# Performance work log

Measured on AMD Instinct MI355X. Metric: run time of the kernel, lower is better.

Reference implementation:

```python
import jax, jax.numpy as jnp
import numpy as np
import math

B, S, D_IN, D_OUT = 4, 2048, 1024, 1024
NEG = -1000000000.0


def setup_inputs() -> dict:
    key = jax.random.key(0)
    ks = jax.random.split(key, 8)
    scale = 1.0 / math.sqrt(D_IN)
    return {
        "x": jax.random.normal(ks[0], (B, S, D_IN), dtype=jnp.float32),
        "Wq": jax.random.normal(ks[1], (D_OUT, D_IN), dtype=jnp.float32) * scale,
        "bq": jax.random.normal(ks[2], (D_OUT,), dtype=jnp.float32) * scale,
        "Wk": jax.random.normal(ks[3], (D_OUT, D_IN), dtype=jnp.float32) * scale,
        "bk": jax.random.normal(ks[4], (D_OUT,), dtype=jnp.float32) * scale,
        "Wv": jax.random.normal(ks[5], (D_OUT, D_IN), dtype=jnp.float32) * scale,
        "bv": jax.random.normal(ks[6], (D_OUT,), dtype=jnp.float32) * scale,
        "lengths": jax.random.randint(ks[7], (B,), 1, S + 1, dtype=jnp.int32),
    }


def reference(x, Wq, bq, Wk, bk, Wv, bv, lengths):
    # QKV projections (self-attention: single input used for q, k, v)
    q = jnp.einsum("bsd,od->bso", x, Wq) + bq
    k = jnp.einsum("bsd,od->bso", x, Wk) + bk
    v = jnp.einsum("bsd,od->bso", x, Wv) + bv
    # scaled scores [B, S, S]
    scores = jnp.einsum("bio,bjo->bij", q, k) / jnp.sqrt(jnp.asarray(D_OUT, q.dtype))
    idx = jnp.arange(S)
    # causal additive mask (mask=True): -1e9 where j > i
    causal = jnp.where(idx[None, :] > idx[:, None], NEG, 0.0).astype(q.dtype)
    # length mask: -1e9 where i >= len[b] or j >= len[b]
    invalid = idx[None, :] >= lengths[:, None]  # [B, S]
    len_mask = jnp.where(invalid[:, :, None] | invalid[:, None, :], NEG, 0.0).astype(q.dtype)
    attn = jax.nn.softmax(scores + causal[None] + len_mask, axis=-1)
    return jnp.einsum("bij,bjo->bio", attn, v)
```

## Files before the change

kernel.cpp:

```cpp
#include <hip/hip_runtime.h>
#include <cstddef>
#include <cstdint>

#define NB 4
#define S_LEN 2048
#define DK 1024

typedef __attribute__((ext_vector_type(8))) short short8;
typedef __attribute__((ext_vector_type(4))) float floatx4;
typedef __attribute__((ext_vector_type(4))) unsigned short ushort4v;
typedef __attribute__((ext_vector_type(8))) unsigned short ushort8v;

__device__ inline unsigned short f2bf(float f) {
    unsigned int u = __float_as_uint(f);
    u += 0x7fff + ((u >> 16) & 1);
    return (unsigned short)(u >> 16);
}
__device__ inline float bf2f(unsigned short u) {
    return __uint_as_float(((unsigned int)u) << 16);
}

#define GLD16(gp, lp)                                                                  \
    __builtin_amdgcn_global_load_lds(                                                  \
        (const __attribute__((address_space(1))) unsigned int*)(gp),                   \
        (__attribute__((address_space(3))) unsigned int*)(lp), 16, 0, 0)

__device__ inline void stage128x64(const unsigned short* __restrict__ g, size_t ld,
                                   unsigned short* __restrict__ lds,
                                   int w, int lane)
{
    const int r8 = lane >> 3;
    const int cg = (lane & 7) ^ r8;
    const unsigned short* gp = g + (size_t)(w * 8 + r8) * ld + cg * 8;
    unsigned short* lp = lds + (size_t)(w * 8) * 64;
    #pragma unroll
    for (int seg = 0; seg < 4; ++seg)
        GLD16(gp + (size_t)(seg * 32) * ld, lp + (size_t)seg * 32 * 64);
}

__global__ __launch_bounds__(256) void cast_all(
    const float* __restrict__ x, const float* __restrict__ Wq,
    const float* __restrict__ Wk, const float* __restrict__ Wv,
    unsigned short* __restrict__ xb, unsigned short* __restrict__ wqb,
    unsigned short* __restrict__ wkb, unsigned short* __restrict__ wvb)
{
    const float* src; unsigned short* dst; int n4;
    if (blockIdx.z == 0)      { src = x;  dst = xb;  n4 = (int)((size_t)NB * S_LEN * DK / 4); }
    else if (blockIdx.z == 1) { src = Wq; dst = wqb; n4 = DK * DK / 4; }
    else if (blockIdx.z == 2) { src = Wk; dst = wkb; n4 = DK * DK / 4; }
    else                      { src = Wv; dst = wvb; n4 = DK * DK / 4; }
    const int stride = gridDim.x * 256;
    for (int i = blockIdx.x * 256 + threadIdx.x; i < n4; i += stride) {
        float4 f = ((const float4*)src)[i];
        ushort4v o;
        o.x = f2bf(f.x); o.y = f2bf(f.y); o.z = f2bf(f.z); o.w = f2bf(f.w);
        ((ushort4v*)dst)[i] = o;
    }
}

__global__ __launch_bounds__(256) void qkv_mfma(
    const unsigned short* __restrict__ xb,
    const unsigned short* __restrict__ wqb, const unsigned short* __restrict__ wkb,
    const unsigned short* __restrict__ wvb,
    const float* __restrict__ bq, const float* __restrict__ bk, const float* __restrict__ bv,
    unsigned short* __restrict__ qb, unsigned short* __restrict__ kb,
    unsigned short* __restrict__ vTb)
{
    __shared__ unsigned short As[128 * 64];
    __shared__ unsigned short Bs[128 * 64];
    const int tid  = threadIdx.x;
    const int w    = tid >> 6, lane = tid & 63;
    const int lm   = lane & 15, quad = lane >> 4;
    const int xr   = lm & 7;
    const int m0   = blockIdx.x * 128, n0 = blockIdx.y * 128;
    const int z    = blockIdx.z;
    const unsigned short* Wb = (z == 0) ? wqb : (z == 1) ? wkb : wvb;
    const float* bias        = (z == 0) ? bq  : (z == 1) ? bk  : bv;

    const unsigned short* Ag = xb + (size_t)m0 * DK;
    const unsigned short* Bg = Wb + (size_t)n0 * DK;

    const int wr = (w >> 1) * 64, wc = (w & 1) * 64;

    floatx4 acc[4][4];
    #pragma unroll
    for (int r = 0; r < 4; ++r)
        #pragma unroll
        for (int c = 0; c < 4; ++c) acc[r][c] = (floatx4)0.0f;

    for (int k0 = 0; k0 < DK; k0 += 64) {
        stage128x64(Ag + k0, DK, As, w, lane);
        stage128x64(Bg + k0, DK, Bs, w, lane);
        __syncthreads();
        #pragma unroll
        for (int ks = 0; ks < 2; ++ks) {
            short8 af[4], bf[4];
            #pragma unroll
            for (int r = 0; r < 4; ++r)
                af[r] = *(const short8*)&As[(size_t)(wr + r*16 + lm) * 64 + ((((ks<<2)|quad) ^ xr) << 3)];
            #pragma unroll
            for (int c = 0; c < 4; ++c)
                bf[c] = *(const short8*)&Bs[(size_t)(wc + c*16 + lm) * 64 + ((((ks<<2)|quad) ^ xr) << 3)];
            #pragma unroll
            for (int r = 0; r < 4; ++r)
                #pragma unroll
                for (int c = 0; c < 4; ++c)
                    acc[r][c] = __builtin_amdgcn_mfma_f32_16x16x32_bf16(af[r], bf[c], acc[r][c], 0, 0, 0);
        }
        __syncthreads();
    }

    if (z < 2) {
        unsigned short* out = (z == 0) ? qb : kb;
        #pragma unroll
        for (int r = 0; r < 4; ++r) {
            const int gm = m0 + wr + r * 16 + quad * 4;
            #pragma unroll
            for (int c = 0; c < 4; ++c) {
                const int gn = n0 + wc + c * 16 + lm;
                const float bb = bias[gn];
                #pragma unroll
                for (int e = 0; e < 4; ++e)
                    out[(size_t)(gm + e) * DK + gn] = f2bf(acc[r][c][e] + bb);
            }
        }
    } else {
        const int bidx = m0 >> 11;
        #pragma unroll
        for (int r = 0; r < 4; ++r) {
            const int gm = m0 + wr + r * 16 + quad * 4;
            const int sm = gm & (S_LEN - 1);
            #pragma unroll
            for (int c = 0; c < 4; ++c) {
                const int gn = n0 + wc + c * 16 + lm;
                const float bb = bias[gn];
                ushort4v pk;
                pk.x = f2bf(acc[r][c][0] + bb);
                pk.y = f2bf(acc[r][c][1] + bb);
                pk.z = f2bf(acc[r][c][2] + bb);
                pk.w = f2bf(acc[r][c][3] + bb);
                *(ushort4v*)&vTb[((size_t)bidx * DK + gn) * S_LEN + sm] = pk;
            }
        }
    }
}

__global__ __launch_bounds__(256) void score_mfma(
    const unsigned short* __restrict__ qb, const unsigned short* __restrict__ kb,
    unsigned short* __restrict__ Pf)
{
    const int bi = blockIdx.x, bj = blockIdx.y, b = blockIdx.z;
    if (bj > bi) return;
    const int m0 = bi * 128, n0 = bj * 128;

    __shared__ unsigned short As[128 * 64];
    __shared__ unsigned short Bs[128 * 64];
    const int tid  = threadIdx.x;
    const int w    = tid >> 6, lane = tid & 63;
    const int lm   = lane & 15, quad = lane >> 4;
    const int xr   = lm & 7;
    const unsigned short* Ag = qb + (size_t)b * S_LEN * DK + (size_t)m0 * DK;
    const unsigned short* Bg = kb + (size_t)b * S_LEN * DK + (size_t)n0 * DK;
    unsigned short* Pb_ = Pf + (size_t)b * S_LEN * S_LEN;

    const int wr = (w >> 1) * 64, wc = (w & 1) * 64;

    floatx4 acc[4][4];
    #pragma unroll
    for (int r = 0; r < 4; ++r)
        #pragma unroll
        for (int c = 0; c < 4; ++c) acc[r][c] = (floatx4)0.0f;

    for (int k0 = 0; k0 < DK; k0 += 64) {
        stage128x64(Ag + k0, DK, As, w, lane);
        stage128x64(Bg + k0, DK, Bs, w, lane);
        __syncthreads();
        #pragma unroll
        for (int ks = 0; ks < 2; ++ks) {
            short8 af[4], bf[4];
            #pragma unroll
            for (int r = 0; r < 4; ++r)
                af[r] = *(const short8*)&As[(size_t)(wr + r*16 + lm) * 64 + ((((ks<<2)|quad) ^ xr) << 3)];
            #pragma unroll
            for (int c = 0; c < 4; ++c)
                bf[c] = *(const short8*)&Bs[(size_t)(wc + c*16 + lm) * 64 + ((((ks<<2)|quad) ^ xr) << 3)];
            #pragma unroll
            for (int r = 0; r < 4; ++r)
                #pragma unroll
                for (int c = 0; c < 4; ++c)
                    acc[r][c] = __builtin_amdgcn_mfma_f32_16x16x32_bf16(af[r], bf[c], acc[r][c], 0, 0, 0);
        }
        __syncthreads();
    }

    #pragma unroll
    for (int r = 0; r < 4; ++r) {
        const int gm = m0 + wr + r * 16 + quad * 4;
        #pragma unroll
        for (int c = 0; c < 4; ++c) {
            const int gn = n0 + wc + c * 16 + lm;
            #pragma unroll
            for (int e = 0; e < 4; ++e)
                Pb_[(size_t)(gm + e) * S_LEN + gn] = f2bf(acc[r][c][e] * 0.03125f);
        }
    }
}

__global__ __launch_bounds__(256) void softmax_rows(
    const unsigned short* __restrict__ Pf, unsigned short* __restrict__ Pb,
    const int* __restrict__ lengths)
{
    const int row = blockIdx.x;
    const int b = row >> 11, i = row & (S_LEN - 1);
    const unsigned short* p = Pf + (size_t)row * S_LEN;
    unsigned short* o = Pb + (size_t)row * S_LEN;
    const int len = lengths[b];
    const int t = threadIdx.x;
    const int nv = i + 1;
    const int j0 = t * 8;

    if (i >= len) {
        const unsigned short u = f2bf(1.0f / (float)nv);
        ushort8v pk;
        #pragma unroll
        for (int e = 0; e < 8; ++e) pk[e] = (j0 + e < nv) ? u : (unsigned short)0;
        *(ushort8v*)&o[j0] = pk;
        return;
    }

    float v[8];
    float m = -INFINITY;
    if (j0 < nv) {
        ushort8v raw = *(const ushort8v*)&p[j0];
        #pragma unroll
        for (int e = 0; e < 8; ++e) {
            float xv = (j0 + e < nv) ? bf2f(raw[e]) : -INFINITY;
            v[e] = xv;
            m = fmaxf(m, xv);
        }
    } else {
        #pragma unroll
        for (int e = 0; e < 8; ++e) v[e] = -INFINITY;
    }

    __shared__ float red[256];
    red[t] = m; __syncthreads();
    #pragma unroll
    for (int s2 = 128; s2 > 0; s2 >>= 1) {
        if (t < s2) red[t] = fmaxf(red[t], red[t + s2]);
        __syncthreads();
    }
    const float M = red[0];
    __syncthreads();

    float s = 0.0f;
    #pragma unroll
    for (int e = 0; e < 8; ++e) {
        if (j0 + e < nv) { v[e] = __expf(v[e] - M); s += v[e]; }
        else v[e] = 0.0f;
    }
    red[t] = s; __syncthreads();
    #pragma unroll
    for (int s2 = 128; s2 > 0; s2 >>= 1) {
        if (t < s2) red[t] += red[t + s2];
        __syncthreads();
    }
    const float inv = 1.0f / red[0];

    ushort8v pk;
    #pragma unroll
    for (int e = 0; e < 8; ++e) pk[e] = f2bf(v[e] * inv);
    *(ushort8v*)&o[j0] = pk;
}

__global__ __launch_bounds__(256) void pv_mfma(
    const unsigned short* __restrict__ Pb, const unsigned short* __restrict__ vTb,
    float* __restrict__ out)
{
    __shared__ unsigned short As[128 * 64];
    __shared__ unsigned short Bs[128 * 64];
    const int tid  = threadIdx.x;
    const int w    = tid >> 6, lane = tid & 63;
    const int lm   = lane & 15, quad = lane >> 4;
    const int xr   = lm & 7;
    const int bi = blockIdx.x, bn = blockIdx.y, b = blockIdx.z;
    const int m0 = bi * 128, n0 = bn * 128;
    const unsigned short* Ag = Pb  + (size_t)b * S_LEN * S_LEN + (size_t)m0 * S_LEN;
    const unsigned short* Bg = vTb + (size_t)b * DK * S_LEN    + (size_t)n0 * S_LEN;

    const int wr = (w >> 1) * 64, wc = (w & 1) * 64;
    const int kend = (bi + 1) * 128;

    floatx4 acc[4][4];
    #pragma unroll
    for (int r = 0; r < 4; ++r)
        #pragma unroll
        for (int c = 0; c < 4; ++c) acc[r][c] = (floatx4)0.0f;

    for (int k0 = 0; k0 < kend; k0 += 64) {
        stage128x64(Ag + k0, S_LEN, As, w, lane);
        stage128x64(Bg + k0, S_LEN, Bs, w, lane);
        __syncthreads();
        #pragma unroll
        for (int ks = 0; ks < 2; ++ks) {
            short8 af[4], bf[4];
            #pragma unroll
            for (int r = 0; r < 4; ++r)
                af[r] = *(const short8*)&As[(size_t)(wr + r*16 + lm) * 64 + ((((ks<<2)|quad) ^ xr) << 3)];
            #pragma unroll
            for (int c = 0; c < 4; ++c)
                bf[c] = *(const short8*)&Bs[(size_t)(wc + c*16 + lm) * 64 + ((((ks<<2)|quad) ^ xr) << 3)];
            #pragma unroll
            for (int r = 0; r < 4; ++r)
                #pragma unroll
                for (int c = 0; c < 4; ++c)
                    acc[r][c] = __builtin_amdgcn_mfma_f32_16x16x32_bf16(af[r], bf[c], acc[r][c], 0, 0, 0);
        }
        __syncthreads();
    }

    #pragma unroll
    for (int r = 0; r < 4; ++r) {
        const int gm = m0 + wr + r * 16 + quad * 4;
        #pragma unroll
        for (int c = 0; c < 4; ++c) {
            const int gn = n0 + wc + c * 16 + lm;
            #pragma unroll
            for (int e = 0; e < 4; ++e)
                out[((size_t)b * S_LEN + gm + e) * DK + gn] = acc[r][c][e];
        }
    }
}

extern "C" void kernel_launch(void* const* d_in, const int* in_sizes, int n_in,
                              void* d_out, int out_size, void* d_ws, size_t ws_size,
                              hipStream_t stream)
{
    const float* x  = (const float*)d_in[0];
    const float* Wq = (const float*)d_in[1];
    const float* bq = (const float*)d_in[2];
    const float* Wk = (const float*)d_in[3];
    const float* bk = (const float*)d_in[4];
    const float* Wv = (const float*)d_in[5];
    const float* bv = (const float*)d_in[6];
    const int* lengths = (const int*)d_in[7];
    float* out = (float*)d_out;

    const size_t NQ = (size_t)NB * S_LEN * DK;
    const size_t NW = (size_t)DK * DK;
    unsigned short* ws16 = (unsigned short*)d_ws;
    unsigned short* qb  = ws16;
    unsigned short* kb_ = ws16 + NQ;
    unsigned short* vTb = ws16 + 2 * NQ;
    unsigned short* xb  = ws16 + 3 * NQ;
    unsigned short* wqb = ws16 + 4 * NQ;
    unsigned short* wkb = wqb + NW;
    unsigned short* wvb = wkb + NW;
    unsigned short* Pf  = ws16 + 4 * NQ + 3 * NW;
    unsigned short* Pb  = ws16;

    cast_all<<<dim3(1024, 1, 4), 256, 0, stream>>>(x, Wq, Wk, Wv, xb, wqb, wkb, wvb);
    qkv_mfma<<<dim3(64, 8, 3), 256, 0, stream>>>(xb, wqb, wkb, wvb, bq, bk, bv, qb, kb_, vTb);
    score_mfma<<<dim3(16, 16, NB), 256, 0, stream>>>(qb, kb_, Pf);
    softmax_rows<<<dim3(NB * S_LEN), 256, 0, stream>>>(Pf, Pb, lengths);
    pv_mfma<<<dim3(16, 8, NB), 256, 0, stream>>>(Pb, vTb, out);
}
```

Baseline: 250.9 us.

## Fuse exp into score kernel and defer softmax normalization to PV epilogue

The score kernel now applies the causal and length masks and writes exp(score) directly, with no running max subtracted. It also launches only lower-triangular tiles through a linearized grid instead of returning early from empty blocks. The softmax pass becomes a row-sum kernel that reads only the causal prefix and stores inverse sums. The PV kernel then scales its output rows by those sums, which removes one full read-write pass over the score matrix. Dropping the max subtraction risks overflow if score magnitudes become large.

```diff
diff --git a/kernel.cpp b/kernel.cpp
--- a/kernel.cpp
+++ b/kernel.cpp
@@ -147,11 +147,15 @@
 
 __global__ __launch_bounds__(256) void score_mfma(
     const unsigned short* __restrict__ qb, const unsigned short* __restrict__ kb,
-    unsigned short* __restrict__ Pf)
-{
-    const int bi = blockIdx.x, bj = blockIdx.y, b = blockIdx.z;
-    if (bj > bi) return;
+    unsigned short* __restrict__ ub, const int* __restrict__ lengths)
+{
+    const int t = blockIdx.x, b = blockIdx.y;
+    int bi = (int)((sqrtf(8.0f * t + 1.0f) - 1.0f) * 0.5f);
+    while ((bi + 1) * (bi + 2) / 2 <= t) ++bi;
+    while (bi * (bi + 1) / 2 > t) --bi;
+    const int bj = t - bi * (bi + 1) / 2;
     const int m0 = bi * 128, n0 = bj * 128;
+    const int len = lengths[b];
 
     __shared__ unsigned short As[128 * 64];
     __shared__ unsigned short Bs[128 * 64];
@@ -161,7 +165,7 @@
     const int xr   = lm & 7;
     const unsigned short* Ag = qb + (size_t)b * S_LEN * DK + (size_t)m0 * DK;
     const unsigned short* Bg = kb + (size_t)b * S_LEN * DK + (size_t)n0 * DK;
-    unsigned short* Pb_ = Pf + (size_t)b * S_LEN * S_LEN;
+    unsigned short* Ub = ub + (size_t)b * S_LEN * S_LEN;
 
     const int wr = (w >> 1) * 64, wc = (w & 1) * 64;
 
@@ -200,82 +204,48 @@
         for (int c = 0; c < 4; ++c) {
             const int gn = n0 + wc + c * 16 + lm;
             #pragma unroll
-            for (int e = 0; e < 4; ++e)
-                Pb_[(size_t)(gm + e) * S_LEN + gn] = f2bf(acc[r][c][e] * 0.03125f);
-        }
-    }
-}
-
-__global__ __launch_bounds__(256) void softmax_rows(
-    const unsigned short* __restrict__ Pf, unsigned short* __restrict__ Pb,
-    const int* __restrict__ lengths)
+            for (int e = 0; e < 4; ++e) {
+                const int i = gm + e;
+                float u;
+                if (gn > i)          u = 0.0f;
+                else if (i >= len)   u = 1.0f;
+                else                 u = __expf(acc[r][c][e] * 0.03125f);
+                Ub[(size_t)i * S_LEN + gn] = f2bf(u);
+            }
+        }
+    }
+}
+
+__global__ __launch_bounds__(256) void row_sum(
+    const unsigned short* __restrict__ ub, float* __restrict__ inv_l)
 {
     const int row = blockIdx.x;
-    const int b = row >> 11, i = row & (S_LEN - 1);
-    const unsigned short* p = Pf + (size_t)row * S_LEN;
-    unsigned short* o = Pb + (size_t)row * S_LEN;
-    const int len = lengths[b];
+    const int i = row & (S_LEN - 1);
+    const int jend = ((i >> 7) + 1) << 7;
+    const unsigned short* p = ub + (size_t)row * S_LEN;
     const int t = threadIdx.x;
-    const int nv = i + 1;
     const int j0 = t * 8;
 
-    if (i >= len) {
-        const unsigned short u = f2bf(1.0f / (float)nv);
-        ushort8v pk;
-        #pragma unroll
-        for (int e = 0; e < 8; ++e) pk[e] = (j0 + e < nv) ? u : (unsigned short)0;
-        *(ushort8v*)&o[j0] = pk;
-        return;
-    }
-
-    float v[8];
-    float m = -INFINITY;
-    if (j0 < nv) {
+    float s = 0.0f;
+    if (j0 < jend) {
         ushort8v raw = *(const ushort8v*)&p[j0];
         #pragma unroll
-        for (int e = 0; e < 8; ++e) {
-            float xv = (j0 + e < nv) ? bf2f(raw[e]) : -INFINITY;
-            v[e] = xv;
-            m = fmaxf(m, xv);
-        }
-    } else {
-        #pragma unroll
-        for (int e = 0; e < 8; ++e) v[e] = -INFINITY;
+        for (int e = 0; e < 8; ++e) s += bf2f(raw[e]);
     }
 
     __shared__ float red[256];
-    red[t] = m; __syncthreads();
-    #pragma unroll
-    for (int s2 = 128; s2 > 0; s2 >>= 1) {
-        if (t < s2) red[t] = fmaxf(red[t], red[t + s2]);
-        __syncthreads();
-    }
-    const float M = red[0];
-    __syncthreads();
-
-    float s = 0.0f;
-    #pragma unroll
-    for (int e = 0; e < 8; ++e) {
-        if (j0 + e < nv) { v[e] = __expf(v[e] - M); s += v[e]; }
-        else v[e] = 0.0f;
-    }
     red[t] = s; __syncthreads();
     #pragma unroll
     for (int s2 = 128; s2 > 0; s2 >>= 1) {
         if (t < s2) red[t] += red[t + s2];
         __syncthreads();
     }
-    const float inv = 1.0f / red[0];
-
-    ushort8v pk;
-    #pragma unroll
-    for (int e = 0; e < 8; ++e) pk[e] = f2bf(v[e] * inv);
-    *(ushort8v*)&o[j0] = pk;
+    if (t == 0) inv_l[row] = 1.0f / red[0];
 }
 
 __global__ __launch_bounds__(256) void pv_mfma(
-    const unsigned short* __restrict__ Pb, const unsigned short* __restrict__ vTb,
-    float* __restrict__ out)
+    const unsigned short* __restrict__ ub, const unsigned short* __restrict__ vTb,
+    const float* __restrict__ inv_l, float* __restrict__ out)
 {
     __shared__ unsigned short As[128 * 64];
     __shared__ unsigned short Bs[128 * 64];
@@ -285,7 +255,7 @@
     const int xr   = lm & 7;
     const int bi = blockIdx.x, bn = blockIdx.y, b = blockIdx.z;
     const int m0 = bi * 128, n0 = bn * 128;
-    const unsigned short* Ag = Pb  + (size_t)b * S_LEN * S_LEN + (size_t)m0 * S_LEN;
+    const unsigned short* Ag = ub  + (size_t)b * S_LEN * S_LEN + (size_t)m0 * S_LEN;
     const unsigned short* Bg = vTb + (size_t)b * DK * S_LEN    + (size_t)n0 * S_LEN;
 
     const int wr = (w >> 1) * 64, wc = (w & 1) * 64;
@@ -322,12 +292,14 @@
     #pragma unroll
     for (int r = 0; r < 4; ++r) {
         const int gm = m0 + wr + r * 16 + quad * 4;
+        const float4 il = *(const float4*)&inv_l[(size_t)b * S_LEN + gm];
+        const float ilv[4] = {il.x, il.y, il.z, il.w};
         #pragma unroll
         for (int c = 0; c < 4; ++c) {
             const int gn = n0 + wc + c * 16 + lm;
             #pragma unroll
             for (int e = 0; e < 4; ++e)
-                out[((size_t)b * S_LEN + gm + e) * DK + gn] = acc[r][c][e];
+                out[((size_t)b * S_LEN + gm + e) * DK + gn] = acc[r][c][e] * ilv[e];
         }
     }
 }
@@ -348,6 +320,7 @@
 
     const size_t NQ = (size_t)NB * S_LEN * DK;
     const size_t NW = (size_t)DK * DK;
+    const size_t NP = (size_t)NB * S_LEN * S_LEN;
     unsigned short* ws16 = (unsigned short*)d_ws;
     unsigned short* qb  = ws16;
     unsigned short* kb_ = ws16 + NQ;
@@ -356,12 +329,12 @@
     unsigned short* wqb = ws16 + 4 * NQ;
     unsigned short* wkb = wqb + NW;
     unsigned short* wvb = wkb + NW;
-    unsigned short* Pf  = ws16 + 4 * NQ + 3 * NW;
-    unsigned short* Pb  = ws16;
+    unsigned short* ub  = ws16 + 4 * NQ + 3 * NW;
+    float* inv_l = (float*)(ub + NP);
 
     cast_all<<<dim3(1024, 1, 4), 256, 0, stream>>>(x, Wq, Wk, Wv, xb, wqb, wkb, wvb);
     qkv_mfma<<<dim3(64, 8, 3), 256, 0, stream>>>(xb, wqb, wkb, wvb, bq, bk, bv, qb, kb_, vTb);
-    score_mfma<<<dim3(16, 16, NB), 256, 0, stream>>>(qb, kb_, Pf);
-    softmax_rows<<<dim3(NB * S_LEN), 256, 0, stream>>>(Pf, Pb, lengths);
-    pv_mfma<<<dim3(16, 8, NB), 256, 0, stream>>>(Pb, vTb, out);
-}
+    score_mfma<<<dim3(136, NB), 256, 0, stream>>>(qb, kb_, ub, lengths);
+    row_sum<<<dim3(NB * S_LEN), 256, 0, stream>>>(ub, inv_l);
+    pv_mfma<<<dim3(16, 8, NB), 256, 0, stream>>>(ub, vTb, inv_l, out);
+}
```

New measurement: 254.1 us. About the same (+1.3%).
